# Performance work log

Hardware: AMD Instinct MI355X
Metric: run time of the kernel (lower is better)

Reference implementation:

```python
import jax, jax.numpy as jnp
import numpy as np

B, S, H = 8, 4096, 1024          # batch, seq_len, hidden_dim
ROUTER_ALPHA = 1.0
CAPACITY = 0.5
K = max(1, int(CAPACITY * S))    # static: active_mask is all-ones -> num_active == S for every row


def setup_inputs() -> dict:
    key = jax.random.key(0)
    k1, k2 = jax.random.split(key)
    hidden_states = jax.random.normal(k1, (B, S, H), dtype=jnp.float32)
    # nn.Linear(H, 1, bias=False) weight, stored as a [H] vector
    w_router = jax.random.normal(k2, (H,), dtype=jnp.float32) / np.sqrt(H).astype(np.float32)
    return {"hidden_states": hidden_states, "w_router": w_router}


def reference(hidden_states, w_router):
    # router projection: [B,S,H] @ [H] -> [B,S]  (Linear(H,1).squeeze(-1))
    router_logits = jnp.einsum('bsh,h->bs', hidden_states, w_router)
    router_scores = jax.nn.sigmoid(router_logits * ROUTER_ALPHA)
    # expert-choice selection: top-K tokens per batch row (K static since mask is all-active)
    _, top_idx = jax.lax.top_k(router_scores, K)              # [B,K]
    selected_mask = jnp.zeros((B, S), dtype=bool).at[
        jnp.arange(B)[:, None], top_idx
    ].set(True)
    router_weights = router_scores * selected_mask.astype(router_scores.dtype)
    return router_weights, selected_mask
```

## Files before the change

kernel.cpp:

```cpp
#include <hip/hip_runtime.h>
#include <math.h>

#define BB 8
#define SS 4096
#define HH 1024
#define KK 2048
#define TOKW 8

__global__ __launch_bounds__(256) void score_kernel(
    const float* __restrict__ hs, const float* __restrict__ w,
    float* __restrict__ scores) {
    const int lane = threadIdx.x & 63;
    const int waveInBlock = threadIdx.x >> 6;
    const long long waveId = (long long)blockIdx.x * 4 + waveInBlock;
    const long long tok0 = waveId * TOKW;

    const float4* w4 = (const float4*)w;
    float4 wf[4];
#pragma unroll
    for (int j = 0; j < 4; ++j) wf[j] = w4[lane + 64 * j];

    const float4* h4 = (const float4*)hs;
#pragma unroll
    for (int t = 0; t < TOKW; ++t) {
        const long long tok = tok0 + t;
        const float4* hrow = h4 + tok * (HH / 4);
        double acc = 0.0;
#pragma unroll
        for (int j = 0; j < 4; ++j) {
            float4 h = hrow[lane + 64 * j];
            acc += (double)h.x * (double)wf[j].x
                 + (double)h.y * (double)wf[j].y
                 + (double)h.z * (double)wf[j].z
                 + (double)h.w * (double)wf[j].w;
        }
#pragma unroll
        for (int off = 32; off >= 1; off >>= 1)
            acc += __shfl_down(acc, off);
        if (lane == 0) {
            double sc = 1.0 / (1.0 + exp(-acc));
            scores[tok] = (float)sc;
        }
    }
}

__global__ __launch_bounds__(256) void select_kernel(
    const float* __restrict__ scores, float* __restrict__ weights,
    float* __restrict__ maskout) {
    const int b = blockIdx.x;
    const int tid = threadIdx.x;
    const float* row = scores + b * SS;

    float v[16];
    unsigned bits[16];
#pragma unroll
    for (int i = 0; i < 16; ++i) {
        v[i] = row[tid * 16 + i];
        bits[i] = __float_as_uint(v[i]);
    }

    __shared__ int red[4];
    __shared__ int scanbuf[256];

    unsigned lo = 0u, hi = 0x3F800001u;
    while (hi - lo > 1u) {
        unsigned mid = lo + ((hi - lo) >> 1);
        int c = 0;
#pragma unroll
        for (int i = 0; i < 16; ++i) c += (bits[i] >= mid) ? 1 : 0;
#pragma unroll
        for (int off = 32; off >= 1; off >>= 1) c += __shfl_down(c, off);
        if ((tid & 63) == 0) red[tid >> 6] = c;
        __syncthreads();
        int total = red[0] + red[1] + red[2] + red[3];
        __syncthreads();
        if (total >= KK) lo = mid; else hi = mid;
    }
    const unsigned thr = lo;

    int cg = 0;
#pragma unroll
    for (int i = 0; i < 16; ++i) cg += (bits[i] > thr) ? 1 : 0;
#pragma unroll
    for (int off = 32; off >= 1; off >>= 1) cg += __shfl_down(cg, off);
    if ((tid & 63) == 0) red[tid >> 6] = cg;
    __syncthreads();
    const int c_gt = red[0] + red[1] + red[2] + red[3];
    __syncthreads();
    const int need = KK - c_gt;

    int ceq = 0;
#pragma unroll
    for (int i = 0; i < 16; ++i) ceq += (bits[i] == thr) ? 1 : 0;
    scanbuf[tid] = ceq;
    __syncthreads();
    if (tid == 0) {
        int run = 0;
        for (int t = 0; t < 256; ++t) {
            int x = scanbuf[t];
            scanbuf[t] = run;
            run += x;
        }
    }
    __syncthreads();

    int run = scanbuf[tid];
#pragma unroll
    for (int i = 0; i < 16; ++i) {
        bool sel;
        if (bits[i] > thr) {
            sel = true;
        } else if (bits[i] == thr) {
            sel = (run < need);
            run++;
        } else {
            sel = false;
        }
        const int idx = b * SS + tid * 16 + i;
        weights[idx] = sel ? v[i] : 0.0f;
        maskout[idx] = sel ? 1.0f : 0.0f;
    }
}

extern "C" void kernel_launch(void* const* d_in, const int* in_sizes, int n_in,
                              void* d_out, int out_size, void* d_ws, size_t ws_size,
                              hipStream_t stream) {
    const float* hs = (const float*)d_in[0];
    const float* w  = (const float*)d_in[1];
    float* out = (float*)d_out;
    float* scores = (float*)d_ws;

    const int tokens = BB * SS;
    const int blocks1 = tokens / (TOKW * 4);
    score_kernel<<<blocks1, 256, 0, stream>>>(hs, w, scores);
    select_kernel<<<BB, 256, 0, stream>>>(scores, out, out + (size_t)BB * SS);
}
```

Baseline: 209.1 us.

## Use one token per wave in scoring and a single-wave select kernel

The score kernel now gives each wave a single token, launching 8192 blocks instead of 1024. It splits the FP64 accumulation into four independent chains and reduces with xor shuffles. The select kernel drops to one 64-lane wave per batch row with float4 loads and stores. That removes all shared-memory reductions and barriers, and replaces the serial single-thread scan with a wave-level shuffle prefix scan. The costs are that the router weight is re-read for every token and each select block has less parallelism for its loads.

```diff
diff --git a/kernel.cpp b/kernel.cpp
--- a/kernel.cpp
+++ b/kernel.cpp
@@ -5,120 +5,109 @@
 #define SS 4096
 #define HH 1024
 #define KK 2048
-#define TOKW 8
 
 __global__ __launch_bounds__(256) void score_kernel(
     const float* __restrict__ hs, const float* __restrict__ w,
     float* __restrict__ scores) {
     const int lane = threadIdx.x & 63;
-    const int waveInBlock = threadIdx.x >> 6;
-    const long long waveId = (long long)blockIdx.x * 4 + waveInBlock;
-    const long long tok0 = waveId * TOKW;
+    const int wv = threadIdx.x >> 6;
+    const int token = blockIdx.x * 4 + wv;
 
     const float4* w4 = (const float4*)w;
-    float4 wf[4];
+    const float4* h4 = (const float4*)(hs + (size_t)token * HH);
+
+    double a0 = 0.0, a1 = 0.0, a2 = 0.0, a3 = 0.0;
 #pragma unroll
-    for (int j = 0; j < 4; ++j) wf[j] = w4[lane + 64 * j];
-
-    const float4* h4 = (const float4*)hs;
+    for (int j = 0; j < 4; ++j) {
+        float4 h  = h4[lane + 64 * j];
+        float4 wf = w4[lane + 64 * j];
+        a0 += (double)h.x * (double)wf.x;
+        a1 += (double)h.y * (double)wf.y;
+        a2 += (double)h.z * (double)wf.z;
+        a3 += (double)h.w * (double)wf.w;
+    }
+    double acc = (a0 + a1) + (a2 + a3);
 #pragma unroll
-    for (int t = 0; t < TOKW; ++t) {
-        const long long tok = tok0 + t;
-        const float4* hrow = h4 + tok * (HH / 4);
-        double acc = 0.0;
-#pragma unroll
-        for (int j = 0; j < 4; ++j) {
-            float4 h = hrow[lane + 64 * j];
-            acc += (double)h.x * (double)wf[j].x
-                 + (double)h.y * (double)wf[j].y
-                 + (double)h.z * (double)wf[j].z
-                 + (double)h.w * (double)wf[j].w;
-        }
-#pragma unroll
-        for (int off = 32; off >= 1; off >>= 1)
-            acc += __shfl_down(acc, off);
-        if (lane == 0) {
-            double sc = 1.0 / (1.0 + exp(-acc));
-            scores[tok] = (float)sc;
-        }
-    }
+    for (int off = 1; off < 64; off <<= 1)
+        acc += __shfl_xor(acc, off);
+    if (lane == 0)
+        scores[token] = (float)(1.0 / (1.0 + exp(-acc)));
 }
 
-__global__ __launch_bounds__(256) void select_kernel(
+__global__ __launch_bounds__(64) void select_kernel(
     const float* __restrict__ scores, float* __restrict__ weights,
     float* __restrict__ maskout) {
     const int b = blockIdx.x;
-    const int tid = threadIdx.x;
-    const float* row = scores + b * SS;
+    const int lane = threadIdx.x;
+    const float4* row4 = (const float4*)(scores + b * SS);
 
-    float v[16];
-    unsigned bits[16];
+    float4 f[16];
 #pragma unroll
-    for (int i = 0; i < 16; ++i) {
-        v[i] = row[tid * 16 + i];
-        bits[i] = __float_as_uint(v[i]);
-    }
-
-    __shared__ int red[4];
-    __shared__ int scanbuf[256];
+    for (int m = 0; m < 16; ++m) f[m] = row4[m * 64 + lane];
 
     unsigned lo = 0u, hi = 0x3F800001u;
     while (hi - lo > 1u) {
-        unsigned mid = lo + ((hi - lo) >> 1);
+        const unsigned mid = lo + ((hi - lo) >> 1);
         int c = 0;
 #pragma unroll
-        for (int i = 0; i < 16; ++i) c += (bits[i] >= mid) ? 1 : 0;
+        for (int m = 0; m < 16; ++m) {
+            c += (__float_as_uint(f[m].x) >= mid);
+            c += (__float_as_uint(f[m].y) >= mid);
+            c += (__float_as_uint(f[m].z) >= mid);
+            c += (__float_as_uint(f[m].w) >= mid);
+        }
 #pragma unroll
-        for (int off = 32; off >= 1; off >>= 1) c += __shfl_down(c, off);
-        if ((tid & 63) == 0) red[tid >> 6] = c;
-        __syncthreads();
-        int total = red[0] + red[1] + red[2] + red[3];
-        __syncthreads();
-        if (total >= KK) lo = mid; else hi = mid;
+        for (int off = 32; off >= 1; off >>= 1) c += __shfl_xor(c, off);
+        if (c >= KK) lo = mid; else hi = mid;
     }
     const unsigned thr = lo;
 
     int cg = 0;
 #pragma unroll
-    for (int i = 0; i < 16; ++i) cg += (bits[i] > thr) ? 1 : 0;
+    for (int m = 0; m < 16; ++m) {
+        cg += (__float_as_uint(f[m].x) > thr);
+        cg += (__float_as_uint(f[m].y) > thr);
+        cg += (__float_as_uint(f[m].z) > thr);
+        cg += (__float_as_uint(f[m].w) > thr);
+    }
 #pragma unroll
-    for (int off = 32; off >= 1; off >>= 1) cg += __shfl_down(cg, off);
-    if ((tid & 63) == 0) red[tid >> 6] = cg;
-    __syncthreads();
-    const int c_gt = red[0] + red[1] + red[2] + red[3];
-    __syncthreads();
-    const int need = KK - c_gt;
+    for (int off = 32; off >= 1; off >>= 1) cg += __shfl_xor(cg, off);
+    const int need = KK - cg;
 
-    int ceq = 0;
+    float4* w4o = (float4*)(weights + b * SS);
+    float4* m4o = (float4*)(maskout + b * SS);
+    int base = 0;
 #pragma unroll
-    for (int i = 0; i < 16; ++i) ceq += (bits[i] == thr) ? 1 : 0;
-    scanbuf[tid] = ceq;
-    __syncthreads();
-    if (tid == 0) {
-        int run = 0;
-        for (int t = 0; t < 256; ++t) {
-            int x = scanbuf[t];
-            scanbuf[t] = run;
-            run += x;
+    for (int m = 0; m < 16; ++m) {
+        const float vals[4] = { f[m].x, f[m].y, f[m].z, f[m].w };
+        unsigned u[4];
+        int eq[4];
+        int ec = 0;
+#pragma unroll
+        for (int c = 0; c < 4; ++c) {
+            u[c] = __float_as_uint(vals[c]);
+            eq[c] = (u[c] == thr) ? 1 : 0;
+            ec += eq[c];
         }
-    }
-    __syncthreads();
-
-    int run = scanbuf[tid];
+        int inc = ec;
 #pragma unroll
-    for (int i = 0; i < 16; ++i) {
-        bool sel;
-        if (bits[i] > thr) {
-            sel = true;
-        } else if (bits[i] == thr) {
-            sel = (run < need);
-            run++;
-        } else {
-            sel = false;
+        for (int off = 1; off < 64; off <<= 1) {
+            int t = __shfl_up(inc, off);
+            if (lane >= off) inc += t;
         }
-        const int idx = b * SS + tid * 16 + i;
-        weights[idx] = sel ? v[i] : 0.0f;
-        maskout[idx] = sel ? 1.0f : 0.0f;
+        const int tot = __shfl(inc, 63);
+        int r = base + inc - ec;
+        float wout[4], mout[4];
+#pragma unroll
+        for (int c = 0; c < 4; ++c) {
+            const bool sel = (u[c] > thr) || (eq[c] && r < need);
+            r += eq[c];
+            wout[c] = sel ? vals[c] : 0.0f;
+            mout[c] = sel ? 1.0f : 0.0f;
+        }
+        base += tot;
+        w4o[m * 64 + lane] = make_float4(wout[0], wout[1], wout[2], wout[3]);
+        m4o[m * 64 + lane] = make_float4(mout[0], mout[1], mout[2], mout[3]);
     }
 }
 
@@ -131,7 +120,6 @@
     float* scores = (float*)d_ws;
 
     const int tokens = BB * SS;
-    const int blocks1 = tokens / (TOKW * 4);
-    score_kernel<<<blocks1, 256, 0, stream>>>(hs, w, scores);
-    select_kernel<<<BB, 256, 0, stream>>>(scores, out, out + (size_t)BB * SS);
+    score_kernel<<<tokens / 4, 256, 0, stream>>>(hs, w, scores);
+    select_kernel<<<BB, 64, 0, stream>>>(scores, out, out + (size_t)BB * SS);
 }
```

Result: no change. 207.6 us (-0.7%).
